# Performance work log

Measured on AMD Instinct MI355X. Metric: run time of the kernel, lower is better.

Reference implementation:

```python
import jax, jax.numpy as jnp
import numpy as np

H = 128
B, N = 8, 200
EPS = 1e-5


def _linear(v, W, b):
    return v @ W.T + b


def _masked_bn(v, m, gamma, beta):
    # v: (..., H); m: (...,) float 0/1 mask. BatchNorm1d over masked rows only
    # (track_running_stats=False -> batch statistics, biased variance).
    mf = m[..., None]
    axes = tuple(range(v.ndim - 1))
    cnt = jnp.maximum(jnp.sum(m), 1.0)
    mean = jnp.sum(v * mf, axis=axes) / cnt            # (H,)
    var = jnp.sum(mf * (v - mean) ** 2, axis=axes) / cnt
    vn = (v - mean) * jax.lax.rsqrt(var + EPS) * gamma + beta
    return jnp.where(mf > 0, vn, v)


def setup_inputs() -> dict:
    key = jax.random.key(0)
    ks = jax.random.split(key, 16)
    s = 1.0 / np.sqrt(H)
    p = lambda k, shp: jax.random.uniform(k, shp, jnp.float32, -s, s)
    return {
        "x": jax.random.normal(ks[0], (B, N, H), jnp.float32),
        "e": jax.random.normal(ks[1], (B, N, N, H), jnp.float32),
        "mask": jax.random.randint(ks[2], (B, N), 0, 2, jnp.int32),
        "Ue_W": p(ks[3], (H, H)), "Ue_b": p(ks[4], (H,)),
        "Ve_W": p(ks[5], (H, H)), "Ve_b": p(ks[6], (H,)),
        "Un_W": p(ks[7], (H, H)), "Un_b": p(ks[8], (H,)),
        "Vn_W": p(ks[9], (H, H)), "Vn_b": p(ks[10], (H,)),
        "bn_n_g": jnp.ones((H,), jnp.float32), "bn_n_b": jnp.zeros((H,), jnp.float32),
        "bn_e_g": jnp.ones((H,), jnp.float32), "bn_e_b": jnp.zeros((H,), jnp.float32),
    }


def reference(x, e, mask, Ue_W, Ue_b, Ve_W, Ve_b, Un_W, Un_b, Vn_W, Vn_b,
              bn_n_g, bn_n_b, bn_e_g, bn_e_b):
    m = mask.astype(x.dtype)                      # (B,N)
    m1 = m[..., None]                             # (B,N,1)
    sq_mask = m[:, :, None] * m[:, None, :]       # (B,N,N)

    # EdgeFeatures: e_ij = U*e_ij + V*x_i + V*x_j (with node-masked Vx)
    Vx = m1 * _linear(x, Ve_W, Ve_b)              # (B,N,H)
    e_tmp = _linear(e, Ue_W, Ue_b) + Vx[:, :, None, :] + Vx[:, None, :, :]

    gate = jax.nn.sigmoid(e_tmp)                  # (B,N,N,H)
    gate_m = gate * sq_mask[..., None]            # mask rows and cols

    # NodeFeatures, sum aggregation: x_i = U*x_i + sum_j gate_ij * (V*x_j)
    Ux = m1 * _linear(x, Un_W, Un_b)
    Vxn = m1 * _linear(x, Vn_W, Vn_b)
    agg = jnp.einsum("bijh,bjh->bih", gate_m, Vxn)
    x_tmp = Ux + agg

    e_bn = _masked_bn(e_tmp, sq_mask, bn_e_g, bn_e_b)
    x_bn = _masked_bn(x_tmp, m, bn_n_g, bn_n_b)

    x_new = x + jax.nn.relu(x_bn)
    e_new = e + jax.nn.relu(e_bn)
    return x_new, e_new
```

## Files before the change

### kernel.cpp

```cpp
#include <hip/hip_runtime.h>
#include <hip/hip_bf16.h>

namespace {

typedef __attribute__((ext_vector_type(8))) short short8;
typedef __attribute__((ext_vector_type(4))) float f32x4;

constexpr int H = 128;
constexpr int N = 200;
constexpr int BN = 1600;
constexpr int X_SIZE = BN * H;
constexpr int NH = N * H;
constexpr long long E_ELEMS = (long long)BN * NH;

constexpr int WS_VX    = 0;
constexpr int WS_UX    = WS_VX + X_SIZE;
constexpr int WS_VXN   = WS_UX + X_SIZE;
constexpr int WS_XTMP  = WS_VXN + X_SIZE;
constexpr int WS_AGG   = WS_XTMP + X_SIZE;
constexpr int WS_ESUMS = WS_AGG + X_SIZE;
constexpr int WS_ESSQS = WS_ESUMS + 32 * H;
constexpr int WS_NSUMS = WS_ESSQS + 32 * H;
constexpr int WS_NSSQS = WS_NSUMS + 8 * H;
constexpr int WS_STAT_END = WS_NSSQS + 8 * H;
constexpr int WS_ESC   = WS_STAT_END;
constexpr int WS_ESH   = WS_ESC + H;
constexpr int WS_NSC   = WS_ESH + H;
constexpr int WS_NSH   = WS_NSC + H;
constexpr int WS_ETMP  = WS_NSH + H;
constexpr size_t NEED_WS_BYTES = (size_t)WS_ETMP * 4 + (size_t)E_ELEMS * 2;

__device__ __forceinline__ unsigned short f2bf(float f) {
  __hip_bfloat16 h = __float2bfloat16(f);
  return __builtin_bit_cast(unsigned short, h);
}

__device__ __forceinline__ short8 pack8(float4 a, float4 b) {
  short8 r;
  r[0] = (short)f2bf(a.x); r[1] = (short)f2bf(a.y);
  r[2] = (short)f2bf(a.z); r[3] = (short)f2bf(a.w);
  r[4] = (short)f2bf(b.x); r[5] = (short)f2bf(b.y);
  r[6] = (short)f2bf(b.z); r[7] = (short)f2bf(b.w);
  return r;
}

__global__ __launch_bounds__(128) void k_prep(
    const float* __restrict__ x, const int* __restrict__ mask,
    const float* __restrict__ VeW, const float* __restrict__ Veb,
    const float* __restrict__ UnW, const float* __restrict__ Unb,
    const float* __restrict__ VnW, const float* __restrict__ Vnb,
    float* __restrict__ ws) {
  const int bi = blockIdx.x, h = threadIdx.x;
  __shared__ float xr[H];
  xr[h] = x[bi * H + h];
  __syncthreads();
  const float mi = (float)mask[bi];
  float a0 = 0.f, a1 = 0.f, a2 = 0.f;
  #pragma unroll 4
  for (int k = 0; k < H; k += 4) {
    const float x0 = xr[k], x1 = xr[k + 1], x2 = xr[k + 2], x3 = xr[k + 3];
    float4 w;
    w = *(const float4*)&VeW[h * H + k];
    a0 += w.x * x0 + w.y * x1 + w.z * x2 + w.w * x3;
    w = *(const float4*)&UnW[h * H + k];
    a1 += w.x * x0 + w.y * x1 + w.z * x2 + w.w * x3;
    w = *(const float4*)&VnW[h * H + k];
    a2 += w.x * x0 + w.y * x1 + w.z * x2 + w.w * x3;
  }
  ws[WS_VX  + bi * H + h] = mi * (a0 + Veb[h]);
  ws[WS_UX  + bi * H + h] = mi * (a1 + Unb[h]);
  ws[WS_VXN + bi * H + h] = mi * (a2 + Vnb[h]);
}

template <int STORE_ETMP>
__global__ __launch_bounds__(256) void k_edge0(
    const float* __restrict__ e, const int* __restrict__ mask,
    const float* __restrict__ UeW, const float* __restrict__ Ueb,
    float* __restrict__ ws, unsigned short* __restrict__ etmp) {
  const int bi = blockIdx.x;
  const int b = bi / N;
  const int tid = threadIdx.x;
  const int w = tid >> 6, lane = tid & 63;
  const int l15 = lane & 15, lg = lane >> 4;
  const int hbase = w * 32;

  __shared__ float etile[2][16 * 128];
  __shared__ float mrow[N];
  __shared__ float pS[4][32], pS2[4][32], pA[4][32];

  if (tid < N) mrow[tid] = (float)mask[b * N + tid];

  const float mi = (float)mask[bi];
  const float* __restrict__ eg = e + (size_t)bi * NH;

  short8 Wf[2][4];
  #pragma unroll
  for (int ht = 0; ht < 2; ++ht) {
    const float* wr = &UeW[(size_t)(hbase + ht * 16 + l15) * H + lg * 8];
    #pragma unroll
    for (int s = 0; s < 4; ++s) {
      const float4 u0 = *(const float4*)(wr + s * 32);
      const float4 u1 = *(const float4*)(wr + s * 32 + 4);
      Wf[ht][s] = pack8(u0, u1);
    }
  }

  float basev[2];
  #pragma unroll
  for (int ht = 0; ht < 2; ++ht) {
    const int h = hbase + ht * 16 + l15;
    basev[ht] = Ueb[h] + ws[WS_VX + (size_t)bi * H + h];
  }

  float bnS[2] = {0.f, 0.f}, bnS2[2] = {0.f, 0.f}, ag[2] = {0.f, 0.f};

  auto stage = [&](int buf, int jt) {
    const int j0 = jt * 16;
    #pragma unroll
    for (int ii = 0; ii < 2; ++ii) {
      const int instr = 2 * w + ii;
      const int row = 2 * instr + (lane >> 5);
      const int c16 = lane & 31;
      const int gr = min(j0 + row, N - 1);
      const int sc16 = c16 ^ (row & 7);
      const float* src = eg + (size_t)gr * H + sc16 * 4;
      float* dst = &etile[buf][instr * 256];
      __builtin_amdgcn_global_load_lds(
          (const __attribute__((address_space(1))) void*)src,
          (__attribute__((address_space(3))) void*)dst, 16, 0, 0);
    }
  };

  stage(0, 0);

  for (int jt = 0; jt < 13; ++jt) {
    const int cur = jt & 1;
    if (jt < 12) stage(cur ^ 1, jt + 1);
    __syncthreads();

    const int j0 = jt * 16;
    const float* tp = &etile[cur][0];

    short8 Ef[4];
    #pragma unroll
    for (int s = 0; s < 4; ++s) {
      const int c0 = (lg * 2 + s * 8) ^ (l15 & 7);
      const int c1 = (lg * 2 + s * 8 + 1) ^ (l15 & 7);
      const float4 u0 = *(const float4*)&tp[l15 * 128 + c0 * 4];
      const float4 u1 = *(const float4*)&tp[l15 * 128 + c1 * 4];
      Ef[s] = pack8(u0, u1);
    }

    f32x4 acc[2] = {f32x4(0.f), f32x4(0.f)};
    #pragma unroll
    for (int s = 0; s < 4; ++s) {
      #pragma unroll
      for (int ht = 0; ht < 2; ++ht)
        acc[ht] = __builtin_amdgcn_mfma_f32_16x16x32_bf16(Ef[s], Wf[ht][s], acc[ht], 0, 0, 0);
    }

    #pragma unroll
    for (int r = 0; r < 4; ++r) {
      const int j = j0 + 4 * lg + r;
      const bool valid = (j < N);
      const int jc = valid ? j : N - 1;
      const float msk = valid ? mi * mrow[jc] : 0.f;
      const size_t row = (size_t)(b * N + jc) * H;
      #pragma unroll
      for (int ht = 0; ht < 2; ++ht) {
        const int h = hbase + ht * 16 + l15;
        const float vx = ws[WS_VX + row + h];
        const float vxn = ws[WS_VXN + row + h];
        const float v = acc[ht][r] + basev[ht] + vx;
        bnS[ht]  += msk * v;
        bnS2[ht] += msk * v * v;
        const float sg = __builtin_amdgcn_rcpf(1.f + __expf(-v));
        ag[ht] += msk * sg * vxn;
        if (STORE_ETMP && valid)
          etmp[(size_t)bi * NH + (size_t)j * H + h] = f2bf(v);
      }
    }
    __syncthreads();
  }

  #pragma unroll
  for (int ht = 0; ht < 2; ++ht) {
    bnS[ht]  += __shfl_xor(bnS[ht], 16);  bnS[ht]  += __shfl_xor(bnS[ht], 32);
    bnS2[ht] += __shfl_xor(bnS2[ht], 16); bnS2[ht] += __shfl_xor(bnS2[ht], 32);
    ag[ht]   += __shfl_xor(ag[ht], 16);   ag[ht]   += __shfl_xor(ag[ht], 32);
  }
  if (lg == 0) {
    #pragma unroll
    for (int ht = 0; ht < 2; ++ht) {
      pS[w][ht * 16 + l15] = bnS[ht];
      pS2[w][ht * 16 + l15] = bnS2[ht];
      pA[w][ht * 16 + l15] = ag[ht];
    }
  }
  __syncthreads();
  if (tid < H) {
    const int w2 = tid >> 5, idx = tid & 31;
    const int slot = (bi & 31) * H + tid;
    atomicAdd(&ws[WS_ESUMS + slot], pS[w2][idx]);
    atomicAdd(&ws[WS_ESSQS + slot], pS2[w2][idx]);
    ws[WS_AGG + (size_t)bi * H + tid] = pA[w2][idx];
  }
}

__global__ void k_x1(const int* __restrict__ mask, float* __restrict__ ws) {
  const int t = blockIdx.x * 256 + threadIdx.x;
  const int h = t & 127, g = t >> 7;
  float s = 0.f, s2 = 0.f;
  for (int bi = g; bi < BN; bi += 100) {
    const float v = ws[WS_UX + bi * H + h] + ws[WS_AGG + bi * H + h];
    ws[WS_XTMP + bi * H + h] = v;
    if (mask[bi] != 0) { s += v; s2 += v * v; }
  }
  atomicAdd(&ws[WS_NSUMS + (g & 7) * H + h], s);
  atomicAdd(&ws[WS_NSSQS + (g & 7) * H + h], s2);
}

__global__ void k_stats(const int* __restrict__ mask,
                        const float* __restrict__ beg, const float* __restrict__ beb,
                        const float* __restrict__ bng, const float* __restrict__ bnb,
                        float* __restrict__ ws) {
  __shared__ float sb[8];
  const int t = threadIdx.x;
  const int b = t >> 5, li = t & 31;
  float s = 0.f;
  for (int i = li; i < N; i += 32) s += (float)mask[b * N + i];
  #pragma unroll
  for (int o = 16; o >= 1; o >>= 1) s += __shfl_down(s, o, 32);
  if (li == 0) sb[b] = s;
  __syncthreads();
  if (t < H) {
    float cn = 0.f, ce = 0.f;
    #pragma unroll
    for (int bb = 0; bb < 8; ++bb) { cn += sb[bb]; ce += sb[bb] * sb[bb]; }
    ce = fmaxf(ce, 1.f); cn = fmaxf(cn, 1.f);
    float es = 0.f, es2 = 0.f;
    #pragma unroll 4
    for (int k = 0; k < 32; ++k) { es += ws[WS_ESUMS + k * H + t]; es2 += ws[WS_ESSQS + k * H + t]; }
    float ns = 0.f, ns2 = 0.f;
    #pragma unroll
    for (int k = 0; k < 8; ++k) { ns += ws[WS_NSUMS + k * H + t]; ns2 += ws[WS_NSSQS + k * H + t]; }
    const float me = es / ce;
    const float ve = fmaxf(es2 / ce - me * me, 0.f);
    const float se = rsqrtf(ve + 1e-5f) * beg[t];
    ws[WS_ESC + t] = se;
    ws[WS_ESH + t] = beb[t] - me * se;
    const float mn = ns / cn;
    const float vn = fmaxf(ns2 / cn - mn * mn, 0.f);
    const float sn = rsqrtf(vn + 1e-5f) * bng[t];
    ws[WS_NSC + t] = sn;
    ws[WS_NSH + t] = bnb[t] - mn * sn;
  }
}

__global__ void k_x2(const float* __restrict__ x, const int* __restrict__ mask,
                     const float* __restrict__ ws, float* __restrict__ out) {
  const int idx = blockIdx.x * 256 + threadIdx.x;
  if (idx >= X_SIZE) return;
  const int h = idx & 127, bi = idx >> 7;
  const float v = ws[WS_XTMP + idx];
  const float r = (mask[bi] != 0) ? (v * ws[WS_NSC + h] + ws[WS_NSH + h]) : v;
  out[idx] = x[idx] + fmaxf(r, 0.f);
}

__global__ __launch_bounds__(256) void k_efin(
    const float* __restrict__ e, const int* __restrict__ mask,
    const float* __restrict__ ws, const unsigned short* __restrict__ etmp,
    float* __restrict__ out) {
  const int t = blockIdx.x * 256 + threadIdx.x;
  const int bi = t / 3200;
  const int rem = t - bi * 3200;
  const int j = rem >> 4;
  const int h0 = (rem & 15) * 8;
  const int b = bi / N;
  const bool on = (mask[bi] & mask[b * N + j]) != 0;

  const size_t base = (size_t)t * 8;
  const ushort4 p0 = *(const ushort4*)&etmp[base];
  const ushort4 p1 = *(const ushort4*)&etmp[base + 4];
  const float4 e0 = *(const float4*)&e[base];
  const float4 e1 = *(const float4*)&e[base + 4];
  const float4 sc0 = *(const float4*)&ws[WS_ESC + h0];
  const float4 sc1 = *(const float4*)&ws[WS_ESC + h0 + 4];
  const float4 sh0 = *(const float4*)&ws[WS_ESH + h0];
  const float4 sh1 = *(const float4*)&ws[WS_ESH + h0 + 4];

  const unsigned short pv[8] = {(unsigned short)p0.x, (unsigned short)p0.y,
                                (unsigned short)p0.z, (unsigned short)p0.w,
                                (unsigned short)p1.x, (unsigned short)p1.y,
                                (unsigned short)p1.z, (unsigned short)p1.w};
  const float ev[8] = {e0.x, e0.y, e0.z, e0.w, e1.x, e1.y, e1.z, e1.w};
  const float scv[8] = {sc0.x, sc0.y, sc0.z, sc0.w, sc1.x, sc1.y, sc1.z, sc1.w};
  const float shv[8] = {sh0.x, sh0.y, sh0.z, sh0.w, sh1.x, sh1.y, sh1.z, sh1.w};

  float o[8];
  #pragma unroll
  for (int k = 0; k < 8; ++k) {
    const float v = __uint_as_float(((unsigned)pv[k]) << 16);
    const float r = on ? (v * scv[k] + shv[k]) : v;
    o[k] = ev[k] + fmaxf(r, 0.f);
  }
  float* og = out + X_SIZE;
  *(float4*)&og[base]     = make_float4(o[0], o[1], o[2], o[3]);
  *(float4*)&og[base + 4] = make_float4(o[4], o[5], o[6], o[7]);
}

__global__ __launch_bounds__(256) void k_erec(
    const float* __restrict__ e, const int* __restrict__ mask,
    const float* __restrict__ UeW, const float* __restrict__ Ueb,
    float* __restrict__ ws, float* __restrict__ out) {
  const int bi = blockIdx.x;
  const int b = bi / N;
  const int tid = threadIdx.x;
  const int w = tid >> 6, lane = tid & 63;
  const int l15 = lane & 15, lg = lane >> 4;
  const int hbase = (w & 1) * 64;

  __shared__ float mrow[N];
  if (tid < N) mrow[tid] = (float)mask[b * N + tid];
  __syncthreads();

  const float mi = (float)mask[bi];
  const float* __restrict__ eg = e + (size_t)bi * NH;

  short8 Wf[4][4];
  #pragma unroll
  for (int ht = 0; ht < 4; ++ht) {
    const float* wr = &UeW[(size_t)(hbase + ht * 16 + l15) * H + lg * 8];
    #pragma unroll
    for (int s = 0; s < 4; ++s) {
      const float4 u0 = *(const float4*)(wr + s * 32);
      const float4 u1 = *(const float4*)(wr + s * 32 + 4);
      Wf[ht][s] = pack8(u0, u1);
    }
  }
  float4 base4[4], sc4[4], sh4[4];
  #pragma unroll
  for (int ht = 0; ht < 4; ++ht) {
    const int h0 = hbase + ht * 16 + 4 * lg;
    const float4 ub = *(const float4*)&Ueb[h0];
    const float4 vx = *(const float4*)&ws[WS_VX + (size_t)bi * H + h0];
    base4[ht] = make_float4(ub.x + vx.x, ub.y + vx.y, ub.z + vx.z, ub.w + vx.w);
    sc4[ht] = *(const float4*)&ws[WS_ESC + h0];
    sh4[ht] = *(const float4*)&ws[WS_ESH + h0];
  }
  const short8 zfrag = {0, 0, 0, 0, 0, 0, 0, 0};
  for (int jt = (w >> 1); jt < 13; jt += 2) {
    const int j0 = jt * 16;
    const int jl = j0 + l15;
    const float* er = eg + (size_t)(jl < N ? jl : 0) * H + lg * 8;
    short8 Ef[4];
    #pragma unroll
    for (int s = 0; s < 4; ++s) {
      const float4 u0 = *(const float4*)(er + s * 32);
      const float4 u1 = *(const float4*)(er + s * 32 + 4);
      Ef[s] = pack8(u0, u1);
    }
    if (jl >= N) {
      #pragma unroll
      for (int s = 0; s < 4; ++s) Ef[s] = zfrag;
    }
    f32x4 acc[4] = {f32x4(0.f), f32x4(0.f), f32x4(0.f), f32x4(0.f)};
    #pragma unroll
    for (int s = 0; s < 4; ++s) {
      #pragma unroll
      for (int ht = 0; ht < 4; ++ht)
        acc[ht] = __builtin_amdgcn_mfma_f32_16x16x32_bf16(Wf[ht][s], Ef[s], acc[ht], 0, 0, 0);
    }
    const int j = j0 + l15;
    if (j < N) {
      const float msk = mi * mrow[j];
      const size_t vrow = (size_t)(b * N + j) * H;
      const size_t erow = (size_t)j * H;
      float* __restrict__ og = out + (size_t)X_SIZE + (size_t)bi * NH + erow;
      #pragma unroll
      for (int ht = 0; ht < 4; ++ht) {
        const int h0 = hbase + ht * 16 + 4 * lg;
        const float4 vx4 = *(const float4*)&ws[WS_VX + vrow + h0];
        const float4 eo4 = *(const float4*)&eg[erow + h0];
        const float vv[4] = {acc[ht][0] + base4[ht].x + vx4.x,
                             acc[ht][1] + base4[ht].y + vx4.y,
                             acc[ht][2] + base4[ht].z + vx4.z,
                             acc[ht][3] + base4[ht].w + vx4.w};
        const float scv[4] = {sc4[ht].x, sc4[ht].y, sc4[ht].z, sc4[ht].w};
        const float shv[4] = {sh4[ht].x, sh4[ht].y, sh4[ht].z, sh4[ht].w};
        const float ev[4] = {eo4.x, eo4.y, eo4.z, eo4.w};
        float o[4];
        #pragma unroll
        for (int r = 0; r < 4; ++r) {
          const float rr = (msk > 0.f) ? (vv[r] * scv[r] + shv[r]) : vv[r];
          o[r] = ev[r] + fmaxf(rr, 0.f);
        }
        *(float4*)&og[h0] = make_float4(o[0], o[1], o[2], o[3]);
      }
    }
  }
}

}

extern "C" void kernel_launch(void* const* d_in, const int* in_sizes, int n_in,
                              void* d_out, int out_size, void* d_ws, size_t ws_size,
                              hipStream_t stream) {
  const float* x    = (const float*)d_in[0];
  const float* e    = (const float*)d_in[1];
  const int*   mask = (const int*)d_in[2];
  const float* UeW  = (const float*)d_in[3];
  const float* Ueb  = (const float*)d_in[4];
  const float* VeW  = (const float*)d_in[5];
  const float* Veb  = (const float*)d_in[6];
  const float* UnW  = (const float*)d_in[7];
  const float* Unb  = (const float*)d_in[8];
  const float* VnW  = (const float*)d_in[9];
  const float* Vnb  = (const float*)d_in[10];
  const float* bng  = (const float*)d_in[11];
  const float* bnb  = (const float*)d_in[12];
  const float* beg  = (const float*)d_in[13];
  const float* beb  = (const float*)d_in[14];
  float* ws  = (float*)d_ws;
  float* out = (float*)d_out;
  unsigned short* etmp = (unsigned short*)(ws + WS_ETMP);
  const bool have_ws = (ws_size >= NEED_WS_BYTES);

  hipMemsetAsync(ws + WS_ESUMS, 0, (WS_STAT_END - WS_ESUMS) * sizeof(float), stream);
  k_prep<<<BN, 128, 0, stream>>>(x, mask, VeW, Veb, UnW, Unb, VnW, Vnb, ws);
  if (have_ws)
    k_edge0<1><<<BN, 256, 0, stream>>>(e, mask, UeW, Ueb, ws, etmp);
  else
    k_edge0<0><<<BN, 256, 0, stream>>>(e, mask, UeW, Ueb, ws, etmp);
  k_x1<<<50, 256, 0, stream>>>(mask, ws);
  k_stats<<<1, 256, 0, stream>>>(mask, beg, beb, bng, bnb, ws);
  k_x2<<<800, 256, 0, stream>>>(x, mask, ws, out);
  if (have_ws)
    k_efin<<<20000, 256, 0, stream>>>(e, mask, ws, etmp, out);
  else
    k_erec<<<BN, 256, 0, stream>>>(e, mask, UeW, Ueb, ws, out);
}
```

Baseline: 232.8 us.

## Recompute edge GEMM in final pass instead of storing bf16 edge intermediate

Drops the bf16 e_tmp buffer and the elementwise finalize kernel. The final pass now recomputes the U*e projection with MFMA and applies batchnorm and the residual directly, removing a large intermediate write and read. The node-aggregation finalization (x_tmp plus its statistics) is fused into the first edge kernel, which also switches from LDS async staging to register double-buffered loads covering a 64-wide h slice per wave. The cost is a second GEMM pass over e and more registers per thread.

```diff
diff --git a/kernel.cpp b/kernel.cpp
--- a/kernel.cpp
+++ b/kernel.cpp
@@ -11,36 +11,32 @@
 constexpr int BN = 1600;
 constexpr int X_SIZE = BN * H;
 constexpr int NH = N * H;
-constexpr long long E_ELEMS = (long long)BN * NH;
 
 constexpr int WS_VX    = 0;
 constexpr int WS_UX    = WS_VX + X_SIZE;
 constexpr int WS_VXN   = WS_UX + X_SIZE;
 constexpr int WS_XTMP  = WS_VXN + X_SIZE;
-constexpr int WS_AGG   = WS_XTMP + X_SIZE;
-constexpr int WS_ESUMS = WS_AGG + X_SIZE;
+constexpr int WS_ESUMS = WS_XTMP + X_SIZE;
 constexpr int WS_ESSQS = WS_ESUMS + 32 * H;
 constexpr int WS_NSUMS = WS_ESSQS + 32 * H;
-constexpr int WS_NSSQS = WS_NSUMS + 8 * H;
-constexpr int WS_STAT_END = WS_NSSQS + 8 * H;
+constexpr int WS_NSSQS = WS_NSUMS + 32 * H;
+constexpr int WS_STAT_END = WS_NSSQS + 32 * H;
 constexpr int WS_ESC   = WS_STAT_END;
 constexpr int WS_ESH   = WS_ESC + H;
 constexpr int WS_NSC   = WS_ESH + H;
 constexpr int WS_NSH   = WS_NSC + H;
-constexpr int WS_ETMP  = WS_NSH + H;
-constexpr size_t NEED_WS_BYTES = (size_t)WS_ETMP * 4 + (size_t)E_ELEMS * 2;
 
 __device__ __forceinline__ unsigned short f2bf(float f) {
   __hip_bfloat16 h = __float2bfloat16(f);
   return __builtin_bit_cast(unsigned short, h);
 }
 
-__device__ __forceinline__ short8 pack8(float4 a, float4 b) {
+__device__ __forceinline__ short8 pack8(f32x4 a, f32x4 b) {
   short8 r;
-  r[0] = (short)f2bf(a.x); r[1] = (short)f2bf(a.y);
-  r[2] = (short)f2bf(a.z); r[3] = (short)f2bf(a.w);
-  r[4] = (short)f2bf(b.x); r[5] = (short)f2bf(b.y);
-  r[6] = (short)f2bf(b.z); r[7] = (short)f2bf(b.w);
+  r[0] = (short)f2bf(a[0]); r[1] = (short)f2bf(a[1]);
+  r[2] = (short)f2bf(a[2]); r[3] = (short)f2bf(a[3]);
+  r[4] = (short)f2bf(b[0]); r[5] = (short)f2bf(b[1]);
+  r[6] = (short)f2bf(b[2]); r[7] = (short)f2bf(b[3]);
   return r;
 }
 
@@ -72,126 +68,111 @@
   ws[WS_VXN + bi * H + h] = mi * (a2 + Vnb[h]);
 }
 
-template <int STORE_ETMP>
-__global__ __launch_bounds__(256) void k_edge0(
+__global__ __launch_bounds__(256, 3) void k_edge0(
     const float* __restrict__ e, const int* __restrict__ mask,
     const float* __restrict__ UeW, const float* __restrict__ Ueb,
-    float* __restrict__ ws, unsigned short* __restrict__ etmp) {
+    float* __restrict__ ws) {
   const int bi = blockIdx.x;
   const int b = bi / N;
   const int tid = threadIdx.x;
   const int w = tid >> 6, lane = tid & 63;
   const int l15 = lane & 15, lg = lane >> 4;
-  const int hbase = w * 32;
-
-  __shared__ float etile[2][16 * 128];
+  const int half = w & 1, pair = w >> 1;
+  const int hbase = half * 64;
+
   __shared__ float mrow[N];
-  __shared__ float pS[4][32], pS2[4][32], pA[4][32];
+  __shared__ float pS[4][64], pS2[4][64], pA[4][64];
 
   if (tid < N) mrow[tid] = (float)mask[b * N + tid];
+  __syncthreads();
 
   const float mi = (float)mask[bi];
   const float* __restrict__ eg = e + (size_t)bi * NH;
 
-  short8 Wf[2][4];
-  #pragma unroll
-  for (int ht = 0; ht < 2; ++ht) {
+  short8 Wf[4][4];
+  #pragma unroll
+  for (int ht = 0; ht < 4; ++ht) {
     const float* wr = &UeW[(size_t)(hbase + ht * 16 + l15) * H + lg * 8];
     #pragma unroll
     for (int s = 0; s < 4; ++s) {
-      const float4 u0 = *(const float4*)(wr + s * 32);
-      const float4 u1 = *(const float4*)(wr + s * 32 + 4);
+      const f32x4 u0 = *(const f32x4*)(wr + s * 32);
+      const f32x4 u1 = *(const f32x4*)(wr + s * 32 + 4);
       Wf[ht][s] = pack8(u0, u1);
     }
   }
 
-  float basev[2];
-  #pragma unroll
-  for (int ht = 0; ht < 2; ++ht) {
+  float basev[4];
+  #pragma unroll
+  for (int ht = 0; ht < 4; ++ht) {
     const int h = hbase + ht * 16 + l15;
     basev[ht] = Ueb[h] + ws[WS_VX + (size_t)bi * H + h];
   }
 
-  float bnS[2] = {0.f, 0.f}, bnS2[2] = {0.f, 0.f}, ag[2] = {0.f, 0.f};
-
-  auto stage = [&](int buf, int jt) {
+  float bnS[4] = {0.f, 0.f, 0.f, 0.f};
+  float bnS2[4] = {0.f, 0.f, 0.f, 0.f};
+  float ag[4] = {0.f, 0.f, 0.f, 0.f};
+
+  auto loadraw = [&](int jt, f32x4* dst) {
+    const int jl = min(jt * 16 + l15, N - 1);
+    const float* er = eg + (size_t)jl * H + lg * 8;
+    #pragma unroll
+    for (int s = 0; s < 4; ++s) {
+      dst[2 * s]     = *(const f32x4*)(er + s * 32);
+      dst[2 * s + 1] = *(const f32x4*)(er + s * 32 + 4);
+    }
+  };
+
+  f32x4 raw[8];
+  loadraw(pair, raw);
+
+  for (int jt = pair; jt < 13; jt += 2) {
+    f32x4 nraw[8];
+    if (jt + 2 < 13) loadraw(jt + 2, nraw);
+
+    short8 Ef[4];
+    #pragma unroll
+    for (int s = 0; s < 4; ++s) Ef[s] = pack8(raw[2 * s], raw[2 * s + 1]);
+
+    f32x4 acc[4] = {f32x4(0.f), f32x4(0.f), f32x4(0.f), f32x4(0.f)};
+    #pragma unroll
+    for (int s = 0; s < 4; ++s) {
+      #pragma unroll
+      for (int ht = 0; ht < 4; ++ht)
+        acc[ht] = __builtin_amdgcn_mfma_f32_16x16x32_bf16(Ef[s], Wf[ht][s], acc[ht], 0, 0, 0);
+    }
+
     const int j0 = jt * 16;
-    #pragma unroll
-    for (int ii = 0; ii < 2; ++ii) {
-      const int instr = 2 * w + ii;
-      const int row = 2 * instr + (lane >> 5);
-      const int c16 = lane & 31;
-      const int gr = min(j0 + row, N - 1);
-      const int sc16 = c16 ^ (row & 7);
-      const float* src = eg + (size_t)gr * H + sc16 * 4;
-      float* dst = &etile[buf][instr * 256];
-      __builtin_amdgcn_global_load_lds(
-          (const __attribute__((address_space(1))) void*)src,
-          (__attribute__((address_space(3))) void*)dst, 16, 0, 0);
-    }
-  };
-
-  stage(0, 0);
-
-  for (int jt = 0; jt < 13; ++jt) {
-    const int cur = jt & 1;
-    if (jt < 12) stage(cur ^ 1, jt + 1);
-    __syncthreads();
-
-    const int j0 = jt * 16;
-    const float* tp = &etile[cur][0];
-
-    short8 Ef[4];
-    #pragma unroll
-    for (int s = 0; s < 4; ++s) {
-      const int c0 = (lg * 2 + s * 8) ^ (l15 & 7);
-      const int c1 = (lg * 2 + s * 8 + 1) ^ (l15 & 7);
-      const float4 u0 = *(const float4*)&tp[l15 * 128 + c0 * 4];
-      const float4 u1 = *(const float4*)&tp[l15 * 128 + c1 * 4];
-      Ef[s] = pack8(u0, u1);
-    }
-
-    f32x4 acc[2] = {f32x4(0.f), f32x4(0.f)};
-    #pragma unroll
-    for (int s = 0; s < 4; ++s) {
-      #pragma unroll
-      for (int ht = 0; ht < 2; ++ht)
-        acc[ht] = __builtin_amdgcn_mfma_f32_16x16x32_bf16(Ef[s], Wf[ht][s], acc[ht], 0, 0, 0);
-    }
-
     #pragma unroll
     for (int r = 0; r < 4; ++r) {
       const int j = j0 + 4 * lg + r;
       const bool valid = (j < N);
       const int jc = valid ? j : N - 1;
       const float msk = valid ? mi * mrow[jc] : 0.f;
-      const size_t row = (size_t)(b * N + jc) * H;
+      const float* rv = &ws[WS_VX + (size_t)(b * N + jc) * H];
+      const float* rn = &ws[WS_VXN + (size_t)(b * N + jc) * H];
       #pragma unroll
-      for (int ht = 0; ht < 2; ++ht) {
+      for (int ht = 0; ht < 4; ++ht) {
         const int h = hbase + ht * 16 + l15;
-        const float vx = ws[WS_VX + row + h];
-        const float vxn = ws[WS_VXN + row + h];
-        const float v = acc[ht][r] + basev[ht] + vx;
+        const float v = acc[ht][r] + basev[ht] + rv[h];
         bnS[ht]  += msk * v;
         bnS2[ht] += msk * v * v;
         const float sg = __builtin_amdgcn_rcpf(1.f + __expf(-v));
-        ag[ht] += msk * sg * vxn;
-        if (STORE_ETMP && valid)
-          etmp[(size_t)bi * NH + (size_t)j * H + h] = f2bf(v);
+        ag[ht] += msk * sg * rn[h];
       }
     }
-    __syncthreads();
-  }
-
-  #pragma unroll
-  for (int ht = 0; ht < 2; ++ht) {
+    #pragma unroll
+    for (int k = 0; k < 8; ++k) raw[k] = nraw[k];
+  }
+
+  #pragma unroll
+  for (int ht = 0; ht < 4; ++ht) {
     bnS[ht]  += __shfl_xor(bnS[ht], 16);  bnS[ht]  += __shfl_xor(bnS[ht], 32);
     bnS2[ht] += __shfl_xor(bnS2[ht], 16); bnS2[ht] += __shfl_xor(bnS2[ht], 32);
     ag[ht]   += __shfl_xor(ag[ht], 16);   ag[ht]   += __shfl_xor(ag[ht], 32);
   }
   if (lg == 0) {
     #pragma unroll
-    for (int ht = 0; ht < 2; ++ht) {
+    for (int ht = 0; ht < 4; ++ht) {
       pS[w][ht * 16 + l15] = bnS[ht];
       pS2[w][ht * 16 + l15] = bnS2[ht];
       pA[w][ht * 16 + l15] = ag[ht];
@@ -199,25 +180,18 @@
   }
   __syncthreads();
   if (tid < H) {
-    const int w2 = tid >> 5, idx = tid & 31;
+    const int hf = tid >> 6, idx = tid & 63;
+    const float s1 = pS[hf][idx] + pS[hf + 2][idx];
+    const float s2 = pS2[hf][idx] + pS2[hf + 2][idx];
+    const float s3 = pA[hf][idx] + pA[hf + 2][idx];
     const int slot = (bi & 31) * H + tid;
-    atomicAdd(&ws[WS_ESUMS + slot], pS[w2][idx]);
-    atomicAdd(&ws[WS_ESSQS + slot], pS2[w2][idx]);
-    ws[WS_AGG + (size_t)bi * H + tid] = pA[w2][idx];
-  }
-}
-
-__global__ void k_x1(const int* __restrict__ mask, float* __restrict__ ws) {
-  const int t = blockIdx.x * 256 + threadIdx.x;
-  const int h = t & 127, g = t >> 7;
-  float s = 0.f, s2 = 0.f;
-  for (int bi = g; bi < BN; bi += 100) {
-    const float v = ws[WS_UX + bi * H + h] + ws[WS_AGG + bi * H + h];
-    ws[WS_XTMP + bi * H + h] = v;
-    if (mask[bi] != 0) { s += v; s2 += v * v; }
-  }
-  atomicAdd(&ws[WS_NSUMS + (g & 7) * H + h], s);
-  atomicAdd(&ws[WS_NSSQS + (g & 7) * H + h], s2);
+    atomicAdd(&ws[WS_ESUMS + slot], s1);
+    atomicAdd(&ws[WS_ESSQS + slot], s2);
+    const float v = ws[WS_UX + (size_t)bi * H + tid] + s3;
+    ws[WS_XTMP + (size_t)bi * H + tid] = v;
+    atomicAdd(&ws[WS_NSUMS + slot], mi * v);
+    atomicAdd(&ws[WS_NSSQS + slot], mi * v * v);
+  }
 }
 
 __global__ void k_stats(const int* __restrict__ mask,
@@ -238,12 +212,14 @@
     #pragma unroll
     for (int bb = 0; bb < 8; ++bb) { cn += sb[bb]; ce += sb[bb] * sb[bb]; }
     ce = fmaxf(ce, 1.f); cn = fmaxf(cn, 1.f);
-    float es = 0.f, es2 = 0.f;
+    float es = 0.f, es2 = 0.f, ns = 0.f, ns2 = 0.f;
     #pragma unroll 4
-    for (int k = 0; k < 32; ++k) { es += ws[WS_ESUMS + k * H + t]; es2 += ws[WS_ESSQS + k * H + t]; }
-    float ns = 0.f, ns2 = 0.f;
-    #pragma unroll
-    for (int k = 0; k < 8; ++k) { ns += ws[WS_NSUMS + k * H + t]; ns2 += ws[WS_NSSQS + k * H + t]; }
+    for (int k = 0; k < 32; ++k) {
+      es  += ws[WS_ESUMS + k * H + t];
+      es2 += ws[WS_ESSQS + k * H + t];
+      ns  += ws[WS_NSUMS + k * H + t];
+      ns2 += ws[WS_NSSQS + k * H + t];
+    }
     const float me = es / ce;
     const float ve = fmaxf(es2 / ce - me * me, 0.f);
     const float se = rsqrtf(ve + 1e-5f) * beg[t];
@@ -267,58 +243,17 @@
   out[idx] = x[idx] + fmaxf(r, 0.f);
 }
 
-__global__ __launch_bounds__(256) void k_efin(
-    const float* __restrict__ e, const int* __restrict__ mask,
-    const float* __restrict__ ws, const unsigned short* __restrict__ etmp,
-    float* __restrict__ out) {
-  const int t = blockIdx.x * 256 + threadIdx.x;
-  const int bi = t / 3200;
-  const int rem = t - bi * 3200;
-  const int j = rem >> 4;
-  const int h0 = (rem & 15) * 8;
-  const int b = bi / N;
-  const bool on = (mask[bi] & mask[b * N + j]) != 0;
-
-  const size_t base = (size_t)t * 8;
-  const ushort4 p0 = *(const ushort4*)&etmp[base];
-  const ushort4 p1 = *(const ushort4*)&etmp[base + 4];
-  const float4 e0 = *(const float4*)&e[base];
-  const float4 e1 = *(const float4*)&e[base + 4];
-  const float4 sc0 = *(const float4*)&ws[WS_ESC + h0];
-  const float4 sc1 = *(const float4*)&ws[WS_ESC + h0 + 4];
-  const float4 sh0 = *(const float4*)&ws[WS_ESH + h0];
-  const float4 sh1 = *(const float4*)&ws[WS_ESH + h0 + 4];
-
-  const unsigned short pv[8] = {(unsigned short)p0.x, (unsigned short)p0.y,
-                                (unsigned short)p0.z, (unsigned short)p0.w,
-                                (unsigned short)p1.x, (unsigned short)p1.y,
-                                (unsigned short)p1.z, (unsigned short)p1.w};
-  const float ev[8] = {e0.x, e0.y, e0.z, e0.w, e1.x, e1.y, e1.z, e1.w};
-  const float scv[8] = {sc0.x, sc0.y, sc0.z, sc0.w, sc1.x, sc1.y, sc1.z, sc1.w};
-  const float shv[8] = {sh0.x, sh0.y, sh0.z, sh0.w, sh1.x, sh1.y, sh1.z, sh1.w};
-
-  float o[8];
-  #pragma unroll
-  for (int k = 0; k < 8; ++k) {
-    const float v = __uint_as_float(((unsigned)pv[k]) << 16);
-    const float r = on ? (v * scv[k] + shv[k]) : v;
-    o[k] = ev[k] + fmaxf(r, 0.f);
-  }
-  float* og = out + X_SIZE;
-  *(float4*)&og[base]     = make_float4(o[0], o[1], o[2], o[3]);
-  *(float4*)&og[base + 4] = make_float4(o[4], o[5], o[6], o[7]);
-}
-
-__global__ __launch_bounds__(256) void k_erec(
+__global__ __launch_bounds__(256, 3) void k_edge1(
     const float* __restrict__ e, const int* __restrict__ mask,
     const float* __restrict__ UeW, const float* __restrict__ Ueb,
-    float* __restrict__ ws, float* __restrict__ out) {
+    const float* __restrict__ ws, float* __restrict__ out) {
   const int bi = blockIdx.x;
   const int b = bi / N;
   const int tid = threadIdx.x;
   const int w = tid >> 6, lane = tid & 63;
   const int l15 = lane & 15, lg = lane >> 4;
-  const int hbase = (w & 1) * 64;
+  const int half = w & 1, pair = w >> 1;
+  const int hbase = half * 64;
 
   __shared__ float mrow[N];
   if (tid < N) mrow[tid] = (float)mask[b * N + tid];
@@ -333,37 +268,42 @@
     const float* wr = &UeW[(size_t)(hbase + ht * 16 + l15) * H + lg * 8];
     #pragma unroll
     for (int s = 0; s < 4; ++s) {
-      const float4 u0 = *(const float4*)(wr + s * 32);
-      const float4 u1 = *(const float4*)(wr + s * 32 + 4);
+      const f32x4 u0 = *(const f32x4*)(wr + s * 32);
+      const f32x4 u1 = *(const f32x4*)(wr + s * 32 + 4);
       Wf[ht][s] = pack8(u0, u1);
     }
   }
-  float4 base4[4], sc4[4], sh4[4];
+
+  f32x4 base4[4];
   #pragma unroll
   for (int ht = 0; ht < 4; ++ht) {
     const int h0 = hbase + ht * 16 + 4 * lg;
-    const float4 ub = *(const float4*)&Ueb[h0];
-    const float4 vx = *(const float4*)&ws[WS_VX + (size_t)bi * H + h0];
-    base4[ht] = make_float4(ub.x + vx.x, ub.y + vx.y, ub.z + vx.z, ub.w + vx.w);
-    sc4[ht] = *(const float4*)&ws[WS_ESC + h0];
-    sh4[ht] = *(const float4*)&ws[WS_ESH + h0];
-  }
-  const short8 zfrag = {0, 0, 0, 0, 0, 0, 0, 0};
-  for (int jt = (w >> 1); jt < 13; jt += 2) {
-    const int j0 = jt * 16;
-    const int jl = j0 + l15;
-    const float* er = eg + (size_t)(jl < N ? jl : 0) * H + lg * 8;
+    const f32x4 ub = *(const f32x4*)&Ueb[h0];
+    const f32x4 vx = *(const f32x4*)&ws[WS_VX + (size_t)bi * H + h0];
+    base4[ht] = ub + vx;
+  }
+
+  auto loadraw = [&](int jt, f32x4* dst) {
+    const int jl = min(jt * 16 + l15, N - 1);
+    const float* er = eg + (size_t)jl * H + lg * 8;
+    #pragma unroll
+    for (int s = 0; s < 4; ++s) {
+      dst[2 * s]     = *(const f32x4*)(er + s * 32);
+      dst[2 * s + 1] = *(const f32x4*)(er + s * 32 + 4);
+    }
+  };
+
+  f32x4 raw[8];
+  loadraw(pair, raw);
+
+  for (int jt = pair; jt < 13; jt += 2) {
+    f32x4 nraw[8];
+    if (jt + 2 < 13) loadraw(jt + 2, nraw);
+
     short8 Ef[4];
     #pragma unroll
-    for (int s = 0; s < 4; ++s) {
-      const float4 u0 = *(const float4*)(er + s * 32);
-      const float4 u1 = *(const float4*)(er + s * 32 + 4);
-      Ef[s] = pack8(u0, u1);
-    }
-    if (jl >= N) {
-      #pragma unroll
-      for (int s = 0; s < 4; ++s) Ef[s] = zfrag;
-    }
+    for (int s = 0; s < 4; ++s) Ef[s] = pack8(raw[2 * s], raw[2 * s + 1]);
+
     f32x4 acc[4] = {f32x4(0.f), f32x4(0.f), f32x4(0.f), f32x4(0.f)};
     #pragma unroll
     for (int s = 0; s < 4; ++s) {
@@ -371,7 +311,8 @@
       for (int ht = 0; ht < 4; ++ht)
         acc[ht] = __builtin_amdgcn_mfma_f32_16x16x32_bf16(Wf[ht][s], Ef[s], acc[ht], 0, 0, 0);
     }
-    const int j = j0 + l15;
+
+    const int j = jt * 16 + l15;
     if (j < N) {
       const float msk = mi * mrow[j];
       const size_t vrow = (size_t)(b * N + j) * H;
@@ -380,24 +321,22 @@
       #pragma unroll
       for (int ht = 0; ht < 4; ++ht) {
         const int h0 = hbase + ht * 16 + 4 * lg;
-        const float4 vx4 = *(const float4*)&ws[WS_VX + vrow + h0];
-        const float4 eo4 = *(const float4*)&eg[erow + h0];
-        const float vv[4] = {acc[ht][0] + base4[ht].x + vx4.x,
-                             acc[ht][1] + base4[ht].y + vx4.y,
-                             acc[ht][2] + base4[ht].z + vx4.z,
-                             acc[ht][3] + base4[ht].w + vx4.w};
-        const float scv[4] = {sc4[ht].x, sc4[ht].y, sc4[ht].z, sc4[ht].w};
-        const float shv[4] = {sh4[ht].x, sh4[ht].y, sh4[ht].z, sh4[ht].w};
-        const float ev[4] = {eo4.x, eo4.y, eo4.z, eo4.w};
-        float o[4];
+        const f32x4 vx4 = *(const f32x4*)&ws[WS_VX + vrow + h0];
+        const f32x4 e4  = *(const f32x4*)&eg[erow + h0];
+        const f32x4 sc4 = *(const f32x4*)&ws[WS_ESC + h0];
+        const f32x4 sh4 = *(const f32x4*)&ws[WS_ESH + h0];
+        f32x4 o;
         #pragma unroll
         for (int r = 0; r < 4; ++r) {
-          const float rr = (msk > 0.f) ? (vv[r] * scv[r] + shv[r]) : vv[r];
-          o[r] = ev[r] + fmaxf(rr, 0.f);
+          const float v = acc[ht][r] + base4[ht][r] + vx4[r];
+          const float rr = (msk > 0.f) ? (v * sc4[r] + sh4[r]) : v;
+          o[r] = e4[r] + fmaxf(rr, 0.f);
         }
-        *(float4*)&og[h0] = make_float4(o[0], o[1], o[2], o[3]);
+        *(f32x4*)&og[h0] = o;
       }
     }
+    #pragma unroll
+    for (int k = 0; k < 8; ++k) raw[k] = nraw[k];
   }
 }
 
@@ -423,20 +362,11 @@
   const float* beb  = (const float*)d_in[14];
   float* ws  = (float*)d_ws;
   float* out = (float*)d_out;
-  unsigned short* etmp = (unsigned short*)(ws + WS_ETMP);
-  const bool have_ws = (ws_size >= NEED_WS_BYTES);
 
   hipMemsetAsync(ws + WS_ESUMS, 0, (WS_STAT_END - WS_ESUMS) * sizeof(float), stream);
   k_prep<<<BN, 128, 0, stream>>>(x, mask, VeW, Veb, UnW, Unb, VnW, Vnb, ws);
-  if (have_ws)
-    k_edge0<1><<<BN, 256, 0, stream>>>(e, mask, UeW, Ueb, ws, etmp);
-  else
-    k_edge0<0><<<BN, 256, 0, stream>>>(e, mask, UeW, Ueb, ws, etmp);
-  k_x1<<<50, 256, 0, stream>>>(mask, ws);
+  k_edge0<<<BN, 256, 0, stream>>>(e, mask, UeW, Ueb, ws);
   k_stats<<<1, 256, 0, stream>>>(mask, beg, beb, bng, bnb, ws);
   k_x2<<<800, 256, 0, stream>>>(x, mask, ws, out);
-  if (have_ws)
-    k_efin<<<20000, 256, 0, stream>>>(e, mask, ws, etmp, out);
-  else
-    k_erec<<<BN, 256, 0, stream>>>(e, mask, UeW, Ueb, ws, out);
-}
+  k_edge1<<<BN, 256, 0, stream>>>(e, mask, UeW, Ueb, ws, out);
+}
```

New measurement: 344.9 us. 48.1% more time.
